# Performance work log

Hardware: AMD Instinct MI355X
Metric: run time of the kernel (lower is better)

Reference implementation:

```python
import jax, jax.numpy as jnp
import numpy as np

N_NODES = 200000
N_EDGES = 200000
N_GRAPHS = 128
IN_FEATS, HID_FEATS, OUT_FEATS = 256, 128, 128


def gcn_conv(x, W, b, src, dst, n_nodes):
    """PyG-style GCNConv: add self-loops, symmetric deg^-1/2 normalization."""
    h = x @ W  # [N, out]
    # degree with self-loops: deg[i] = 1 + (# edges with target i)
    deg = 1.0 + jax.ops.segment_sum(jnp.ones(src.shape[0], x.dtype), dst,
                                    num_segments=n_nodes)
    dinv = jax.lax.rsqrt(deg)
    norm = dinv[src] * dinv[dst]  # per-edge coeff
    agg = jax.ops.segment_sum(h[src] * norm[:, None], dst, num_segments=n_nodes)
    agg = agg + h * (1.0 / deg)[:, None]  # self-loop contribution
    return agg + b


def setup_inputs() -> dict:
    key = jax.random.key(0)
    k = jax.random.split(key, 8)
    x = jax.random.normal(k[0], (N_NODES, IN_FEATS), jnp.float32)
    edge_index = jax.random.randint(k[1], (2, N_EDGES), 0, N_NODES)
    batch = jnp.sort(jax.random.randint(k[2], (N_NODES,), 0, N_GRAPHS))
    root_index = jax.random.randint(k[3], (N_GRAPHS,), 0, N_NODES)
    # GCNConv params (xavier-ish scale)
    W1 = jax.random.normal(k[4], (IN_FEATS, HID_FEATS), jnp.float32) * (2.0 / (IN_FEATS + HID_FEATS)) ** 0.5
    b1 = jnp.zeros((HID_FEATS,), jnp.float32)
    W2 = jax.random.normal(k[5], (HID_FEATS + IN_FEATS, OUT_FEATS), jnp.float32) * (2.0 / (HID_FEATS + IN_FEATS + OUT_FEATS)) ** 0.5
    b2 = jnp.zeros((OUT_FEATS,), jnp.float32)
    return {"x": x, "edge_index": edge_index, "batch": batch,
            "root_index": root_index, "W1": W1, "b1": b1, "W2": W2, "b2": b2}


def reference(x, edge_index, batch, root_index, W1, b1, W2, b2):
    src, dst = edge_index[0], edge_index[1]
    x1 = x  # raw input features
    h = gcn_conv(x, W1, b1, src, dst, N_NODES)  # conv1 -> [N, hid]
    x2 = h
    # root broadcast: root_extend[i] = x1[root_index[batch[i]]]
    root_extend = x1[root_index[batch]]  # [N, in]
    h = jnp.concatenate([h, root_extend], axis=1)  # [N, hid+in]
    h = jax.nn.relu(h)
    # F.dropout(training=self.training): eval mode -> identity
    h = gcn_conv(h, W2, b2, src, dst, N_NODES)  # conv2 -> [N, out]
    h = jax.nn.relu(h)
    root_extend2 = x2[root_index[batch]]  # [N, hid]
    h = jnp.concatenate([h, root_extend2], axis=1)  # [N, out+hid]
    # scatter_mean over graphs
    sums = jax.ops.segment_sum(h, batch, num_segments=N_GRAPHS)
    counts = jax.ops.segment_sum(jnp.ones((N_NODES,), h.dtype), batch,
                                 num_segments=N_GRAPHS)
    return sums / jnp.maximum(counts, 1.0)[:, None]  # [B, out+hid]
```

## Files before the change

kernel.cpp:

```cpp
#include <hip/hip_runtime.h>
#include <stddef.h>

constexpr int N_NODES = 200000;
constexpr int N_EDGES = 200000;
constexpr int N_GRAPHS = 128;
constexpr int IN_F = 256;
constexpr int HID_F = 128;
constexpr int OUT_F = 128;
constexpr int OUT_W = OUT_F + HID_F;
constexpr int SCAN_NB = (N_NODES + 1023) / 1024;
constexpr int EDGE_NB = (N_EDGES + 255) / 256;
constexpr int CHUNKS = 128;

typedef __attribute__((ext_vector_type(8))) short short8;
typedef __attribute__((ext_vector_type(4))) float float4v;

__device__ __forceinline__ short f2bf(float f) {
    union { float f; unsigned u; } v; v.f = f;
    unsigned r = v.u + 0x7fffu + ((v.u >> 16) & 1u);
    return (short)(r >> 16);
}
__device__ __forceinline__ float bf2f(unsigned short s) {
    union { unsigned u; float f; } v; v.u = ((unsigned)s) << 16;
    return v.f;
}

__global__ __launch_bounds__(256) void init_kernel(
    const int* __restrict__ batch, const float* __restrict__ W1,
    const float* __restrict__ W2,
    int* __restrict__ cursor, float* __restrict__ rootlin,
    int* __restrict__ startv, int* __restrict__ cntg,
    short* __restrict__ Bt1, short* __restrict__ Bt2)
{
    __shared__ int s_start[N_GRAPHS + 1];
    const int t = threadIdx.x;
    const int gid = blockIdx.x * 256 + t;

    if (gid < N_NODES) cursor[gid] = 0;
    if (gid < N_GRAPHS * OUT_F) rootlin[gid] = 0.f;
    if (gid < 128 * IN_F) {
        int n = gid >> 8, k = gid & 255;
        Bt1[(size_t)n * IN_F + k] = f2bf(W1[(size_t)k * 128 + n]);
    } else if (gid < 128 * IN_F + 128 * HID_F) {
        int tw = gid - 128 * IN_F;
        int n = tw >> 7, k = tw & 127;
        Bt2[(size_t)n * HID_F + k] = f2bf(W2[(size_t)k * 128 + n]);
    }
    if (blockIdx.x == 0) {
        if (t <= N_GRAPHS) {
            int g = t, lo = 0, hi = N_NODES;
            while (lo < hi) {
                int mid = (lo + hi) >> 1;
                if (batch[mid] < g) lo = mid + 1; else hi = mid;
            }
            s_start[t] = lo;
        }
        __syncthreads();
        if (t < N_GRAPHS) {
            startv[t] = s_start[t];
            cntg[t] = s_start[t + 1] - s_start[t];
        }
    }
}

__global__ void edge_prep_kernel(const int* __restrict__ dst, int* __restrict__ cntin, int E) {
    int e = blockIdx.x * blockDim.x + threadIdx.x;
    if (e < E) atomicAdd(&cntin[dst[e]], 1);
}

__global__ __launch_bounds__(1024) void scan_reduce_kernel(const int* __restrict__ cnt,
                                                           int* __restrict__ partial, int n) {
    __shared__ int sm[1024];
    int t = threadIdx.x;
    int i = blockIdx.x * 1024 + t;
    sm[t] = (i < n) ? cnt[i] : 0;
    __syncthreads();
    for (int ofs = 512; ofs > 0; ofs >>= 1) {
        if (t < ofs) sm[t] += sm[t + ofs];
        __syncthreads();
    }
    if (t == 0) partial[blockIdx.x] = sm[0];
}

__global__ void scan_base_kernel(int* __restrict__ partial, int nb) {
    __shared__ int sm[256];
    int t = threadIdx.x;
    sm[t] = (t < nb) ? partial[t] : 0;
    __syncthreads();
    for (int ofs = 1; ofs < 256; ofs <<= 1) {
        int v = (t >= ofs) ? sm[t - ofs] : 0;
        __syncthreads();
        sm[t] += v;
        __syncthreads();
    }
    if (t < nb) partial[t] = (t == 0) ? 0 : sm[t - 1];
}

__global__ __launch_bounds__(1024) void scan_final_kernel(const int* __restrict__ cnt,
                                                          const int* __restrict__ partial,
                                                          int* __restrict__ rp,
                                                          int* __restrict__ cur,
                                                          float* __restrict__ dinv, int n) {
    __shared__ int sm[1024];
    int t = threadIdx.x;
    int i = blockIdx.x * 1024 + t;
    int v = (i < n) ? cnt[i] : 0;
    sm[t] = v;
    __syncthreads();
    for (int ofs = 1; ofs < 1024; ofs <<= 1) {
        int u = (t >= ofs) ? sm[t - ofs] : 0;
        __syncthreads();
        sm[t] += u;
        __syncthreads();
    }
    int base = partial[blockIdx.x];
    if (i < n) {
        int ex = base + sm[t] - v;
        rp[i] = ex;
        cur[i] = ex;
        dinv[i] = rsqrtf(1.0f + (float)v);
        if (i == n - 1) rp[n] = ex + v;
    }
}

__global__ __launch_bounds__(256) void bucket_rootlin_kernel(
    const int* __restrict__ src, const int* __restrict__ dst,
    int* __restrict__ cur, int* __restrict__ adj,
    const float* __restrict__ x, const int* __restrict__ root_index,
    const float* __restrict__ W2, float* __restrict__ rootlin)
{
    int b = blockIdx.x;
    int t = threadIdx.x;
    if (b < EDGE_NB) {
        int e = b * 256 + t;
        if (e < N_EDGES) {
            int pos = atomicAdd(&cur[dst[e]], 1);
            adj[pos] = src[e];
        }
    } else {
        int rb = b - EDGE_NB;
        int g = rb >> 1;
        int f = t & 127;
        int k0 = (rb & 1) * 128 + (t >> 7) * 64;
        int r = root_index[g];
        const float* xr = x + (size_t)r * IN_F;
        float acc = 0.f;
        for (int k = k0; k < k0 + 64; ++k)
            acc += fmaxf(xr[k], 0.f) * W2[(size_t)(HID_F + k) * OUT_F + f];
        atomicAdd(&rootlin[(size_t)g * OUT_F + f], acc);
    }
}

__global__ __launch_bounds__(256) void agg2_kernel(
    const unsigned short* __restrict__ hs1, const float* __restrict__ dinv,
    const float* __restrict__ b1v, const int* __restrict__ rp,
    const int* __restrict__ adj, unsigned short* __restrict__ hsag)
{
    int gid = blockIdx.x * 256 + threadIdx.x;
    int r = gid >> 3;
    int c0 = (gid & 7) * 16;
    const unsigned short* hp = hs1 + (size_t)r * 128 + c0;
    float sum[16];
    {
        short8 h0 = *(const short8*)hp;
        short8 h1 = *(const short8*)(hp + 8);
        #pragma unroll
        for (int q = 0; q < 8; ++q) {
            sum[q] = bf2f((unsigned short)h0[q]);
            sum[8 + q] = bf2f((unsigned short)h1[q]);
        }
    }
    int e0 = rp[r], e1 = rp[r + 1];
    for (int e = e0; e < e1; ++e) {
        const unsigned short* qp = hs1 + (size_t)adj[e] * 128 + c0;
        short8 h0 = *(const short8*)qp;
        short8 h1 = *(const short8*)(qp + 8);
        #pragma unroll
        for (int q = 0; q < 8; ++q) {
            sum[q] += bf2f((unsigned short)h0[q]);
            sum[8 + q] += bf2f((unsigned short)h1[q]);
        }
    }
    float di = dinv[r];
    short8 s0, s1;
    #pragma unroll
    for (int q = 0; q < 8; ++q) {
        s0[q] = f2bf(fmaxf(di * sum[q] + b1v[c0 + q], 0.f));
        s1[q] = f2bf(fmaxf(di * sum[8 + q] + b1v[c0 + 8 + q], 0.f));
    }
    unsigned short* op = hsag + (size_t)r * 128 + c0;
    *(short8*)op = s0;
    *(short8*)(op + 8) = s1;
}

template<int KTOT, bool ABF16, bool ADDROOT>
__global__ __launch_bounds__(256, 4) void mfma_gemm_kernel(
    const void* __restrict__ Ap, const short* __restrict__ Bt,
    unsigned short* __restrict__ outp,
    const float* __restrict__ dinv,
    const float* __restrict__ rootlin, const int* __restrict__ batch)
{
    __shared__ __align__(16) short Bs[128][136];

    const int tid = threadIdx.x;
    const int wave = tid >> 6;
    const int lane = tid & 63;
    const int quad = lane >> 4;
    const int l16  = lane & 15;
    const int row0 = blockIdx.x * 64;
    const int arow = row0 + wave * 16 + l16;

    float4v acc[8];
    #pragma unroll
    for (int c = 0; c < 8; ++c) acc[c] = (float4v){0.f, 0.f, 0.f, 0.f};

    const int bn = tid >> 1;
    const int bk = (tid & 1) * 64;
    constexpr int NKB = KTOT / 128;

    for (int kb = 0; kb < NKB; ++kb) {
        {
            const short* bp = Bt + (size_t)bn * KTOT + kb * 128 + bk;
            #pragma unroll
            for (int j = 0; j < 8; ++j)
                *(short8*)&Bs[bn][bk + 8 * j] = *(const short8*)(bp + 8 * j);
        }
        __syncthreads();
        #pragma unroll
        for (int ks = 0; ks < 4; ++ks) {
            short8 af;
            if (ABF16) {
                const unsigned short* ap = (const unsigned short*)Ap
                    + (size_t)arow * KTOT + kb * 128 + ks * 32 + quad * 8;
                af = *(const short8*)ap;
            } else {
                const float* ap = (const float*)Ap
                    + (size_t)arow * KTOT + kb * 128 + ks * 32 + quad * 8;
                float4 f0 = *(const float4*)ap;
                float4 f1 = *(const float4*)(ap + 4);
                af[0] = f2bf(f0.x); af[1] = f2bf(f0.y); af[2] = f2bf(f0.z); af[3] = f2bf(f0.w);
                af[4] = f2bf(f1.x); af[5] = f2bf(f1.y); af[6] = f2bf(f1.z); af[7] = f2bf(f1.w);
            }
            #pragma unroll
            for (int c = 0; c < 8; ++c) {
                short8 bf = *(const short8*)&Bs[c * 16 + l16][ks * 32 + quad * 8];
                acc[c] = __builtin_amdgcn_mfma_f32_16x16x32_bf16(af, bf, acc[c], 0, 0, 0);
            }
        }
        if (kb + 1 < NKB) __syncthreads();
    }

    #pragma unroll
    for (int r = 0; r < 4; ++r) {
        int row = row0 + wave * 16 + quad * 4 + r;
        float di = dinv[row];
        const float* rl = nullptr;
        if (ADDROOT) rl = rootlin + (size_t)batch[row] * 128;
        #pragma unroll
        for (int c = 0; c < 8; ++c) {
            int col = c * 16 + l16;
            float v = acc[c][r];
            if (ADDROOT) v += rl[col];
            outp[(size_t)row * 128 + col] = (unsigned short)f2bf(v * di);
        }
    }
}

__global__ void mean_kernel(const unsigned short* __restrict__ hs2,
                            const unsigned short* __restrict__ hs1,
                            const float* __restrict__ dinv, const float* __restrict__ b1v,
                            const float* __restrict__ b2v, const int* __restrict__ root_index,
                            const int* __restrict__ cnt, const int* __restrict__ start,
                            const int* __restrict__ rp, const int* __restrict__ adj,
                            float* __restrict__ pmean, float* __restrict__ out)
{
    int g = blockIdx.x;
    int c = blockIdx.y;
    int f = threadIdx.x;
    int s = start[g], n = cnt[g];
    int per = (n + CHUNKS - 1) / CHUNKS;
    int lo = s + c * per;
    int hi = min(s + n, lo + per);
    float bb = b2v[f];
    float accv = 0.f;
    for (int i = lo; i < hi; ++i) {
        float v = bf2f(hs2[(size_t)i * 128 + f]);
        int e0 = rp[i], e1 = rp[i + 1];
        for (int e = e0; e < e1; ++e)
            v += bf2f(hs2[(size_t)adj[e] * 128 + f]);
        accv += fmaxf(dinv[i] * v + bb, 0.f);
    }
    pmean[(size_t)c * (N_GRAPHS * 128) + g * 128 + f] = accv;
    if (c == 0) {
        int r = root_index[g];
        float v = 0.f;
        if (n > 0) {
            v = bf2f(hs1[(size_t)r * 128 + f]);
            int e0 = rp[r], e1 = rp[r + 1];
            for (int e = e0; e < e1; ++e)
                v += bf2f(hs1[(size_t)adj[e] * 128 + f]);
            v = dinv[r] * v + b1v[f];
        }
        out[(size_t)g * OUT_W + HID_F + f] = v;
    }
}

__global__ void meanreduce_kernel(const float* __restrict__ pmean,
                                  const int* __restrict__ cnt,
                                  float* __restrict__ out)
{
    int g = blockIdx.x;
    int f = threadIdx.x;
    float s = 0.f;
    for (int c = 0; c < CHUNKS; ++c)
        s += pmean[(size_t)c * (N_GRAPHS * 128) + g * 128 + f];
    out[(size_t)g * OUT_W + f] = s / (float)max(cnt[g], 1);
}


static inline size_t align_up(size_t x, size_t a) { return (x + a - 1) / a * a; }

extern "C" void kernel_launch(void* const* d_in, const int* in_sizes, int n_in,
                              void* d_out, int out_size, void* d_ws, size_t ws_size,
                              hipStream_t stream) {
    const float* x = (const float*)d_in[0];
    const int* ei = (const int*)d_in[1];
    const int* batch = (const int*)d_in[2];
    const int* root = (const int*)d_in[3];
    const float* W1 = (const float*)d_in[4];
    const float* b1 = (const float*)d_in[5];
    const float* W2 = (const float*)d_in[6];
    const float* b2 = (const float*)d_in[7];
    float* out = (float*)d_out;

    const int* src = ei;
    const int* dst = ei + N_EDGES;

    char* ws = (char*)d_ws;
    size_t off = 0;
    const size_t NB16 = (size_t)N_NODES * 128 * sizeof(unsigned short);

    float* dinv = (float*)(ws + off);    off = align_up(off + (size_t)N_NODES * sizeof(float), 256);
    int* cntg = (int*)(ws + off);        off = align_up(off + N_GRAPHS * sizeof(int), 256);
    int* startv = (int*)(ws + off);      off = align_up(off + N_GRAPHS * sizeof(int), 256);
    float* rootlin = (float*)(ws + off); off = align_up(off + (size_t)N_GRAPHS * OUT_F * sizeof(float), 256);
    short* Bt1 = (short*)(ws + off);     off = align_up(off + (size_t)128 * IN_F * sizeof(short), 256);
    short* Bt2 = (short*)(ws + off);     off = align_up(off + (size_t)128 * HID_F * sizeof(short), 256);
    int* rowptr = (int*)(ws + off);      off = align_up(off + (size_t)(N_NODES + 1) * sizeof(int), 256);
    int* cursor = (int*)(ws + off);      off = align_up(off + (size_t)N_NODES * sizeof(int), 256);
    int* partial = (int*)(ws + off);     off = align_up(off + (size_t)SCAN_NB * sizeof(int), 256);
    int* adj = (int*)(ws + off);         off = align_up(off + (size_t)N_EDGES * sizeof(int), 256);
    float* pmean = (float*)(ws + off);   off = align_up(off + (size_t)CHUNKS * N_GRAPHS * 128 * sizeof(float), 256);
    unsigned short* hs1 = (unsigned short*)(ws + off);  off = align_up(off + NB16, 256);
    unsigned short* hs2 = (unsigned short*)(ws + off);  off = align_up(off + NB16, 256);
    unsigned short* hsag = (unsigned short*)(ws + off); off = align_up(off + NB16, 256);
    (void)ws_size; (void)n_in; (void)in_sizes; (void)out_size;

    init_kernel<<<EDGE_NB, 256, 0, stream>>>(batch, W1, W2, cursor, rootlin,
                                             startv, cntg, Bt1, Bt2);
    edge_prep_kernel<<<EDGE_NB, 256, 0, stream>>>(dst, cursor, N_EDGES);
    scan_reduce_kernel<<<SCAN_NB, 1024, 0, stream>>>(cursor, partial, N_NODES);
    scan_base_kernel<<<1, 256, 0, stream>>>(partial, SCAN_NB);
    scan_final_kernel<<<SCAN_NB, 1024, 0, stream>>>(cursor, partial, rowptr, cursor, dinv, N_NODES);
    bucket_rootlin_kernel<<<EDGE_NB + 2 * N_GRAPHS, 256, 0, stream>>>(
        src, dst, cursor, adj, x, root, W2, rootlin);

    mfma_gemm_kernel<IN_F, false, false><<<N_NODES / 64, 256, 0, stream>>>(
        x, Bt1, hs1, dinv, nullptr, nullptr);

    agg2_kernel<<<(N_NODES * 8) / 256, 256, 0, stream>>>(hs1, dinv, b1, rowptr, adj, hsag);

    mfma_gemm_kernel<HID_F, true, true><<<N_NODES / 64, 256, 0, stream>>>(
        hsag, Bt2, hs2, dinv, rootlin, batch);

    dim3 mg(N_GRAPHS, CHUNKS);
    mean_kernel<<<mg, 128, 0, stream>>>(hs2, hs1, dinv, b1, b2, root, cntg, startv,
                                        rowptr, adj, pmean, out);
    meanreduce_kernel<<<N_GRAPHS, 128, 0, stream>>>(pmean, cntg, out);
}
```

Measured before the change: 479.7 us.

## Fuse layer-1 aggregation into conv2 GEMM, vectorize mean kernel, drop scan base

The conv1 neighbor aggregation, bias and ReLU are now computed directly in the A-fragment registers of the conv2 MFMA kernel. This removes the separate agg2 kernel and the bf16 intermediate buffer write and read. The mean kernel now loads 8 features per thread with short8 vector loads across 8 row lanes and reduces through shared memory. The scan_base kernel is removed: each scan_final block sums the preceding partials itself. The costs are higher register pressure in the fused GEMM and a serial prefix loop per scan block.

Result: faster. 441.7 us (-7.9%).

```diff
diff --git a/kernel.cpp b/kernel.cpp
--- a/kernel.cpp
+++ b/kernel.cpp
@@ -82,28 +82,16 @@
     if (t == 0) partial[blockIdx.x] = sm[0];
 }
 
-__global__ void scan_base_kernel(int* __restrict__ partial, int nb) {
-    __shared__ int sm[256];
-    int t = threadIdx.x;
-    sm[t] = (t < nb) ? partial[t] : 0;
-    __syncthreads();
-    for (int ofs = 1; ofs < 256; ofs <<= 1) {
-        int v = (t >= ofs) ? sm[t - ofs] : 0;
-        __syncthreads();
-        sm[t] += v;
-        __syncthreads();
-    }
-    if (t < nb) partial[t] = (t == 0) ? 0 : sm[t - 1];
-}
-
 __global__ __launch_bounds__(1024) void scan_final_kernel(const int* __restrict__ cnt,
                                                           const int* __restrict__ partial,
                                                           int* __restrict__ rp,
                                                           int* __restrict__ cur,
                                                           float* __restrict__ dinv, int n) {
     __shared__ int sm[1024];
+    __shared__ int pb[SCAN_NB];
     int t = threadIdx.x;
     int i = blockIdx.x * 1024 + t;
+    if (t < SCAN_NB) pb[t] = partial[t];
     int v = (i < n) ? cnt[i] : 0;
     sm[t] = v;
     __syncthreads();
@@ -113,7 +101,8 @@
         sm[t] += u;
         __syncthreads();
     }
-    int base = partial[blockIdx.x];
+    int base = 0;
+    for (int j = 0; j < blockIdx.x; ++j) base += pb[j];
     if (i < n) {
         int ex = base + sm[t] - v;
         rp[i] = ex;
@@ -151,54 +140,9 @@
     }
 }
 
-__global__ __launch_bounds__(256) void agg2_kernel(
-    const unsigned short* __restrict__ hs1, const float* __restrict__ dinv,
-    const float* __restrict__ b1v, const int* __restrict__ rp,
-    const int* __restrict__ adj, unsigned short* __restrict__ hsag)
-{
-    int gid = blockIdx.x * 256 + threadIdx.x;
-    int r = gid >> 3;
-    int c0 = (gid & 7) * 16;
-    const unsigned short* hp = hs1 + (size_t)r * 128 + c0;
-    float sum[16];
-    {
-        short8 h0 = *(const short8*)hp;
-        short8 h1 = *(const short8*)(hp + 8);
-        #pragma unroll
-        for (int q = 0; q < 8; ++q) {
-            sum[q] = bf2f((unsigned short)h0[q]);
-            sum[8 + q] = bf2f((unsigned short)h1[q]);
-        }
-    }
-    int e0 = rp[r], e1 = rp[r + 1];
-    for (int e = e0; e < e1; ++e) {
-        const unsigned short* qp = hs1 + (size_t)adj[e] * 128 + c0;
-        short8 h0 = *(const short8*)qp;
-        short8 h1 = *(const short8*)(qp + 8);
-        #pragma unroll
-        for (int q = 0; q < 8; ++q) {
-            sum[q] += bf2f((unsigned short)h0[q]);
-            sum[8 + q] += bf2f((unsigned short)h1[q]);
-        }
-    }
-    float di = dinv[r];
-    short8 s0, s1;
-    #pragma unroll
-    for (int q = 0; q < 8; ++q) {
-        s0[q] = f2bf(fmaxf(di * sum[q] + b1v[c0 + q], 0.f));
-        s1[q] = f2bf(fmaxf(di * sum[8 + q] + b1v[c0 + 8 + q], 0.f));
-    }
-    unsigned short* op = hsag + (size_t)r * 128 + c0;
-    *(short8*)op = s0;
-    *(short8*)(op + 8) = s1;
-}
-
-template<int KTOT, bool ABF16, bool ADDROOT>
-__global__ __launch_bounds__(256, 4) void mfma_gemm_kernel(
-    const void* __restrict__ Ap, const short* __restrict__ Bt,
-    unsigned short* __restrict__ outp,
-    const float* __restrict__ dinv,
-    const float* __restrict__ rootlin, const int* __restrict__ batch)
+__global__ __launch_bounds__(256, 4) void conv1_kernel(
+    const float* __restrict__ Ap, const short* __restrict__ Bt,
+    unsigned short* __restrict__ outp, const float* __restrict__ dinv)
 {
     __shared__ __align__(16) short Bs[128][136];
 
@@ -216,9 +160,9 @@
 
     const int bn = tid >> 1;
     const int bk = (tid & 1) * 64;
-    constexpr int NKB = KTOT / 128;
-
-    for (int kb = 0; kb < NKB; ++kb) {
+    constexpr int KTOT = IN_F;
+
+    for (int kb = 0; kb < 2; ++kb) {
         {
             const short* bp = Bt + (size_t)bn * KTOT + kb * 128 + bk;
             #pragma unroll
@@ -228,80 +172,182 @@
         __syncthreads();
         #pragma unroll
         for (int ks = 0; ks < 4; ++ks) {
+            const float* ap = Ap + (size_t)arow * KTOT + kb * 128 + ks * 32 + quad * 8;
+            float4 f0 = *(const float4*)ap;
+            float4 f1 = *(const float4*)(ap + 4);
             short8 af;
-            if (ABF16) {
-                const unsigned short* ap = (const unsigned short*)Ap
-                    + (size_t)arow * KTOT + kb * 128 + ks * 32 + quad * 8;
-                af = *(const short8*)ap;
-            } else {
-                const float* ap = (const float*)Ap
-                    + (size_t)arow * KTOT + kb * 128 + ks * 32 + quad * 8;
-                float4 f0 = *(const float4*)ap;
-                float4 f1 = *(const float4*)(ap + 4);
-                af[0] = f2bf(f0.x); af[1] = f2bf(f0.y); af[2] = f2bf(f0.z); af[3] = f2bf(f0.w);
-                af[4] = f2bf(f1.x); af[5] = f2bf(f1.y); af[6] = f2bf(f1.z); af[7] = f2bf(f1.w);
-            }
+            af[0] = f2bf(f0.x); af[1] = f2bf(f0.y); af[2] = f2bf(f0.z); af[3] = f2bf(f0.w);
+            af[4] = f2bf(f1.x); af[5] = f2bf(f1.y); af[6] = f2bf(f1.z); af[7] = f2bf(f1.w);
             #pragma unroll
             for (int c = 0; c < 8; ++c) {
                 short8 bf = *(const short8*)&Bs[c * 16 + l16][ks * 32 + quad * 8];
                 acc[c] = __builtin_amdgcn_mfma_f32_16x16x32_bf16(af, bf, acc[c], 0, 0, 0);
             }
         }
-        if (kb + 1 < NKB) __syncthreads();
+        if (kb == 0) __syncthreads();
     }
 
     #pragma unroll
     for (int r = 0; r < 4; ++r) {
         int row = row0 + wave * 16 + quad * 4 + r;
         float di = dinv[row];
-        const float* rl = nullptr;
-        if (ADDROOT) rl = rootlin + (size_t)batch[row] * 128;
+        #pragma unroll
+        for (int c = 0; c < 8; ++c)
+            outp[(size_t)row * 128 + c * 16 + l16] = (unsigned short)f2bf(acc[c][r] * di);
+    }
+}
+
+__global__ __launch_bounds__(256, 4) void conv2_fused_kernel(
+    const unsigned short* __restrict__ hs1, const short* __restrict__ Bt,
+    unsigned short* __restrict__ hs2,
+    const float* __restrict__ dinv, const float* __restrict__ b1v,
+    const float* __restrict__ rootlin, const int* __restrict__ batch,
+    const int* __restrict__ rp, const int* __restrict__ adj)
+{
+    __shared__ __align__(16) short Bs[128][136];
+
+    const int tid = threadIdx.x;
+    const int wave = tid >> 6;
+    const int lane = tid & 63;
+    const int quad = lane >> 4;
+    const int l16  = lane & 15;
+    const int row0 = blockIdx.x * 64;
+    const int arow = row0 + wave * 16 + l16;
+
+    {
+        const int bn = tid >> 1;
+        const int bk = (tid & 1) * 64;
+        const short* bp = Bt + (size_t)bn * HID_F + bk;
+        #pragma unroll
+        for (int j = 0; j < 8; ++j)
+            *(short8*)&Bs[bn][bk + 8 * j] = *(const short8*)(bp + 8 * j);
+    }
+
+    float sum[4][8];
+    {
+        const unsigned short* hp = hs1 + (size_t)arow * 128 + quad * 8;
+        #pragma unroll
+        for (int ks = 0; ks < 4; ++ks) {
+            short8 h = *(const short8*)(hp + ks * 32);
+            #pragma unroll
+            for (int q = 0; q < 8; ++q) sum[ks][q] = bf2f((unsigned short)h[q]);
+        }
+        int e0 = rp[arow], e1 = rp[arow + 1];
+        for (int e = e0; e < e1; ++e) {
+            const unsigned short* qp = hs1 + (size_t)adj[e] * 128 + quad * 8;
+            #pragma unroll
+            for (int ks = 0; ks < 4; ++ks) {
+                short8 h = *(const short8*)(qp + ks * 32);
+                #pragma unroll
+                for (int q = 0; q < 8; ++q) sum[ks][q] += bf2f((unsigned short)h[q]);
+            }
+        }
+    }
+    float di_a = dinv[arow];
+    short8 af[4];
+    #pragma unroll
+    for (int ks = 0; ks < 4; ++ks) {
+        const float* bv = b1v + quad * 8 + ks * 32;
+        #pragma unroll
+        for (int q = 0; q < 8; ++q)
+            af[ks][q] = f2bf(fmaxf(di_a * sum[ks][q] + bv[q], 0.f));
+    }
+
+    __syncthreads();
+
+    float4v acc[8];
+    #pragma unroll
+    for (int c = 0; c < 8; ++c) acc[c] = (float4v){0.f, 0.f, 0.f, 0.f};
+    #pragma unroll
+    for (int ks = 0; ks < 4; ++ks) {
+        #pragma unroll
+        for (int c = 0; c < 8; ++c) {
+            short8 bf = *(const short8*)&Bs[c * 16 + l16][ks * 32 + quad * 8];
+            acc[c] = __builtin_amdgcn_mfma_f32_16x16x32_bf16(af[ks], bf, acc[c], 0, 0, 0);
+        }
+    }
+
+    #pragma unroll
+    for (int r = 0; r < 4; ++r) {
+        int row = row0 + wave * 16 + quad * 4 + r;
+        float di = dinv[row];
+        const float* rl = rootlin + (size_t)batch[row] * 128;
         #pragma unroll
         for (int c = 0; c < 8; ++c) {
             int col = c * 16 + l16;
-            float v = acc[c][r];
-            if (ADDROOT) v += rl[col];
-            outp[(size_t)row * 128 + col] = (unsigned short)f2bf(v * di);
-        }
-    }
-}
-
-__global__ void mean_kernel(const unsigned short* __restrict__ hs2,
-                            const unsigned short* __restrict__ hs1,
-                            const float* __restrict__ dinv, const float* __restrict__ b1v,
-                            const float* __restrict__ b2v, const int* __restrict__ root_index,
-                            const int* __restrict__ cnt, const int* __restrict__ start,
-                            const int* __restrict__ rp, const int* __restrict__ adj,
-                            float* __restrict__ pmean, float* __restrict__ out)
-{
+            hs2[(size_t)row * 128 + col] = (unsigned short)f2bf((acc[c][r] + rl[col]) * di);
+        }
+    }
+}
+
+__global__ __launch_bounds__(128) void mean_kernel(
+    const unsigned short* __restrict__ hs2, const unsigned short* __restrict__ hs1,
+    const float* __restrict__ dinv, const float* __restrict__ b1v,
+    const float* __restrict__ b2v, const int* __restrict__ root_index,
+    const int* __restrict__ cnt, const int* __restrict__ start,
+    const int* __restrict__ rp, const int* __restrict__ adj,
+    float* __restrict__ pmean, float* __restrict__ out)
+{
+    __shared__ float sm[8][128];
     int g = blockIdx.x;
     int c = blockIdx.y;
-    int f = threadIdx.x;
+    int t = threadIdx.x;
+    int wv = t >> 6;
+    int lane = t & 63;
+    int sub = lane >> 4;
+    int l16 = lane & 15;
+    int c0 = l16 * 8;
+
     int s = start[g], n = cnt[g];
     int per = (n + CHUNKS - 1) / CHUNKS;
     int lo = s + c * per;
     int hi = min(s + n, lo + per);
-    float bb = b2v[f];
-    float accv = 0.f;
-    for (int i = lo; i < hi; ++i) {
-        float v = bf2f(hs2[(size_t)i * 128 + f]);
+
+    float bb[8];
+    #pragma unroll
+    for (int q = 0; q < 8; ++q) bb[q] = b2v[c0 + q];
+
+    float accv[8];
+    #pragma unroll
+    for (int q = 0; q < 8; ++q) accv[q] = 0.f;
+
+    for (int i = lo + wv * 4 + sub; i < hi; i += 8) {
+        float v[8];
+        short8 h = *(const short8*)(hs2 + (size_t)i * 128 + c0);
+        #pragma unroll
+        for (int q = 0; q < 8; ++q) v[q] = bf2f((unsigned short)h[q]);
         int e0 = rp[i], e1 = rp[i + 1];
-        for (int e = e0; e < e1; ++e)
-            v += bf2f(hs2[(size_t)adj[e] * 128 + f]);
-        accv += fmaxf(dinv[i] * v + bb, 0.f);
-    }
-    pmean[(size_t)c * (N_GRAPHS * 128) + g * 128 + f] = accv;
+        for (int e = e0; e < e1; ++e) {
+            short8 ha = *(const short8*)(hs2 + (size_t)adj[e] * 128 + c0);
+            #pragma unroll
+            for (int q = 0; q < 8; ++q) v[q] += bf2f((unsigned short)ha[q]);
+        }
+        float di = dinv[i];
+        #pragma unroll
+        for (int q = 0; q < 8; ++q) accv[q] += fmaxf(di * v[q] + bb[q], 0.f);
+    }
+
+    #pragma unroll
+    for (int q = 0; q < 8; ++q) sm[wv * 4 + sub][c0 + q] = accv[q];
+    __syncthreads();
+    {
+        float s2 = 0.f;
+        #pragma unroll
+        for (int r = 0; r < 8; ++r) s2 += sm[r][t];
+        pmean[(size_t)c * (N_GRAPHS * 128) + g * 128 + t] = s2;
+    }
+
     if (c == 0) {
         int r = root_index[g];
         float v = 0.f;
         if (n > 0) {
-            v = bf2f(hs1[(size_t)r * 128 + f]);
+            v = bf2f(hs1[(size_t)r * 128 + t]);
             int e0 = rp[r], e1 = rp[r + 1];
             for (int e = e0; e < e1; ++e)
-                v += bf2f(hs1[(size_t)adj[e] * 128 + f]);
-            v = dinv[r] * v + b1v[f];
-        }
-        out[(size_t)g * OUT_W + HID_F + f] = v;
+                v += bf2f(hs1[(size_t)adj[e] * 128 + t]);
+            v = dinv[r] * v + b1v[t];
+        }
+        out[(size_t)g * OUT_W + HID_F + t] = v;
     }
 }
 
@@ -353,25 +399,20 @@
     float* pmean = (float*)(ws + off);   off = align_up(off + (size_t)CHUNKS * N_GRAPHS * 128 * sizeof(float), 256);
     unsigned short* hs1 = (unsigned short*)(ws + off);  off = align_up(off + NB16, 256);
     unsigned short* hs2 = (unsigned short*)(ws + off);  off = align_up(off + NB16, 256);
-    unsigned short* hsag = (unsigned short*)(ws + off); off = align_up(off + NB16, 256);
     (void)ws_size; (void)n_in; (void)in_sizes; (void)out_size;
 
     init_kernel<<<EDGE_NB, 256, 0, stream>>>(batch, W1, W2, cursor, rootlin,
                                              startv, cntg, Bt1, Bt2);
     edge_prep_kernel<<<EDGE_NB, 256, 0, stream>>>(dst, cursor, N_EDGES);
     scan_reduce_kernel<<<SCAN_NB, 1024, 0, stream>>>(cursor, partial, N_NODES);
-    scan_base_kernel<<<1, 256, 0, stream>>>(partial, SCAN_NB);
     scan_final_kernel<<<SCAN_NB, 1024, 0, stream>>>(cursor, partial, rowptr, cursor, dinv, N_NODES);
     bucket_rootlin_kernel<<<EDGE_NB + 2 * N_GRAPHS, 256, 0, stream>>>(
         src, dst, cursor, adj, x, root, W2, rootlin);
 
-    mfma_gemm_kernel<IN_F, false, false><<<N_NODES / 64, 256, 0, stream>>>(
-        x, Bt1, hs1, dinv, nullptr, nullptr);
-
-    agg2_kernel<<<(N_NODES * 8) / 256, 256, 0, stream>>>(hs1, dinv, b1, rowptr, adj, hsag);
-
-    mfma_gemm_kernel<HID_F, true, true><<<N_NODES / 64, 256, 0, stream>>>(
-        hsag, Bt2, hs2, dinv, rootlin, batch);
+    conv1_kernel<<<N_NODES / 64, 256, 0, stream>>>(x, Bt1, hs1, dinv);
+
+    conv2_fused_kernel<<<N_NODES / 64, 256, 0, stream>>>(
+        hs1, Bt2, hs2, dinv, b1, rootlin, batch, rowptr, adj);
 
     dim3 mg(N_GRAPHS, CHUNKS);
     mean_kernel<<<mg, 128, 0, stream>>>(hs2, hs1, dinv, b1, b2, root, cntg, startv,
```
